# Optimization experiments

Measured on AMD Instinct MI355X. Metric: run time of the kernel, lower is better.

Reference implementation:

```python
import jax, jax.numpy as jnp
import numpy as np
from jax import lax

B, H, W, C = 16, 32, 32, 256
HEADS = 8
HD = C // HEADS          # attention_head_dim = 32
KSZ = 3                  # conv_kernel_size
DIL = 2                  # dilation_rate
SCALE = HD ** -0.5


def setup_inputs() -> dict:
    key = jax.random.key(0)
    k0, k1, k2, k3 = jax.random.split(key, 4)
    return {
        "query": jax.random.normal(k0, (B, H, W, C), jnp.float32),
        "key_in": jax.random.normal(k1, (B, H, W, C), jnp.float32),
        "value": jax.random.normal(k2, (B, H, W, C), jnp.float32),
        # depthwise conv: kernel [kh, kw, in_ch/groups=1, out_ch=C], plus bias [C]
        "conv_kernel": jax.random.normal(k3, (KSZ, KSZ, 1, C), jnp.float32) * 0.05,
        "conv_bias": jnp.zeros((C,), jnp.float32),
    }


def _dwconv(x, kernel, bias):
    # depthwise dilated conv, padding SAME (Keras Conv2D groups=C)
    y = lax.conv_general_dilated(
        x, kernel,
        window_strides=(1, 1), padding="SAME",
        rhs_dilation=(DIL, DIL),
        dimension_numbers=("NHWC", "HWIO", "NHWC"),
        feature_group_count=C,
    )
    return y + bias


def _to_heads(x):
    # [B,H,W,C] -> [B, heads, S, head_dim]
    return x.reshape(B, H * W, HEADS, HD).transpose(0, 2, 1, 3)


def reference(query, key_in, value, conv_kernel, conv_bias):
    q = _to_heads(query)
    k = _to_heads(_dwconv(key_in, conv_kernel, conv_bias))
    v = _to_heads(_dwconv(value, conv_kernel, conv_bias))
    scores = jnp.einsum("bhqd,bhkd->bhqk", q, k) * SCALE  # [B,heads,S,S]
    attn = jax.nn.softmax(scores, axis=-1)
    out = jnp.einsum("bhqk,bhkd->bhqd", attn, v)          # [B,heads,S,hd]
    return out.transpose(0, 2, 1, 3).reshape(B, H, W, C)
```

## Files before the change

### kernel.cpp

```cpp
#include <hip/hip_runtime.h>

#define B_    16
#define HH    32
#define WW    32
#define CC    256
#define HEADS 8
#define HD    32
#define S_    1024
#define KT    128
#define NITER (S_ / KT)
#define SCALE_L2E 0.25503486f

typedef unsigned short u16;
typedef unsigned int   u32;
typedef __attribute__((ext_vector_type(8))) short short8;
typedef __attribute__((ext_vector_type(4))) float f32x4;

__device__ __forceinline__ u16 f2bf(float f) {
    u32 x = __float_as_uint(f);
    return (u16)((x + 0x7fffu + ((x >> 16) & 1u)) >> 16);
}
__device__ __forceinline__ u32 pack2bf(float lo, float hi) {
    return (u32)f2bf(lo) | ((u32)f2bf(hi) << 16);
}

__global__ __launch_bounds__(256) void dw_conv_kernel(
    const float* __restrict__ key_in, const float* __restrict__ value,
    const float* __restrict__ ck, const float* __restrict__ cb,
    u16* __restrict__ Kws, u16* __restrict__ Vws)
{
    int idx = blockIdx.x * 256 + threadIdx.x;
    int c4 = idx & 63;
    int x  = (idx >> 6) & 31;
    int y  = (idx >> 11) & 31;
    int b  = (idx >> 16) & 15;
    int t  = idx >> 20;
    const float* __restrict__ src = t ? value : key_in;

    float4 acc = *(const float4*)(cb + 4 * c4);
    #pragma unroll
    for (int kh = 0; kh < 3; kh++) {
        int yy = y + kh * 2 - 2;
        if (yy < 0 || yy >= HH) continue;
        #pragma unroll
        for (int kw = 0; kw < 3; kw++) {
            int xx = x + kw * 2 - 2;
            if (xx < 0 || xx >= WW) continue;
            float4 w = *(const float4*)(ck + (kh * 3 + kw) * CC + 4 * c4);
            size_t ii = ((((size_t)b * HH + yy) * WW) + xx) * CC + 4 * c4;
            float4 v = *(const float4*)(src + ii);
            acc.x += w.x * v.x; acc.y += w.y * v.y;
            acc.z += w.z * v.z; acc.w += w.w * v.w;
        }
    }

    int h = c4 >> 3;
    int d = (c4 & 7) * 4;
    int s = y * WW + x;
    size_t o = (((size_t)(b * HEADS + h)) * S_ + s) * HD + d;
    if (t == 0) {
        *(uint2*)&Kws[o] = make_uint2(pack2bf(acc.x * SCALE_L2E, acc.y * SCALE_L2E),
                                      pack2bf(acc.z * SCALE_L2E, acc.w * SCALE_L2E));
    } else {
        *(uint2*)&Vws[o] = make_uint2(pack2bf(acc.x, acc.y), pack2bf(acc.z, acc.w));
    }
}

__global__ __launch_bounds__(256, 4) void attn_kernel(
    const float* __restrict__ query,
    const u16* __restrict__ Kws, const u16* __restrict__ Vws,
    float* __restrict__ out)
{
    __shared__ __align__(16) u16 Vtlds[2][HD][KT + 8];

    const int tid  = threadIdx.x;
    const int lane = tid & 63;
    const int wv   = tid >> 6;
    const int q15  = lane & 15;
    const int quad = lane >> 4;

    const int blk = blockIdx.x;
    const int bh  = blk & 127;
    const int qt  = blk >> 7;
    const int b = bh >> 3, h = bh & 7;
    const int q0w = qt * 128 + wv * 32;

    short8 qf[2];
    #pragma unroll
    for (int f = 0; f < 2; f++) {
        const float* qp = query + ((size_t)(b * S_ + q0w + f * 16 + q15)) * CC
                          + h * HD + quad * 8;
        float4 a = *(const float4*)(qp);
        float4 c = *(const float4*)(qp + 4);
        short8 v;
        v[0] = (short)f2bf(a.x); v[1] = (short)f2bf(a.y);
        v[2] = (short)f2bf(a.z); v[3] = (short)f2bf(a.w);
        v[4] = (short)f2bf(c.x); v[5] = (short)f2bf(c.y);
        v[6] = (short)f2bf(c.z); v[7] = (short)f2bf(c.w);
        qf[f] = v;
    }

    short8 ones;
    #pragma unroll
    for (int j = 0; j < 8; j++) ones[j] = (short)0x3F80;

    const u16* Kg = Kws + (size_t)bh * S_ * HD;
    const u16* Vg = Vws + (size_t)bh * S_ * HD;

    const int vg  = tid >> 3, vs4 = tid & 7;
    const int vc = vg >> 3, vw = vg & 7;
    const int vt2 = (vw >> 2) & 1, vqd = vw & 3;
    const int vpg = (vc << 5) | (vqd << 3) | (vt2 << 2);

    uint2 vr0, vr1, vr2, vr3;

    auto issue_v_loads = [&](int kt0) {
        const uint2* vsrc = (const uint2*)(Vg + (size_t)(kt0 + 4 * vg) * HD + 4 * vs4);
        vr0 = vsrc[0]; vr1 = vsrc[8]; vr2 = vsrc[16]; vr3 = vsrc[24];
    };
    auto write_lds = [&](int p) {
        u32 a, bb;
        a  = __builtin_amdgcn_perm(vr1.x, vr0.x, 0x05040100u);
        bb = __builtin_amdgcn_perm(vr3.x, vr2.x, 0x05040100u);
        *(uint2*)&Vtlds[p][4 * vs4 + 0][vpg] = make_uint2(a, bb);
        a  = __builtin_amdgcn_perm(vr1.x, vr0.x, 0x07060302u);
        bb = __builtin_amdgcn_perm(vr3.x, vr2.x, 0x07060302u);
        *(uint2*)&Vtlds[p][4 * vs4 + 1][vpg] = make_uint2(a, bb);
        a  = __builtin_amdgcn_perm(vr1.y, vr0.y, 0x05040100u);
        bb = __builtin_amdgcn_perm(vr3.y, vr2.y, 0x05040100u);
        *(uint2*)&Vtlds[p][4 * vs4 + 2][vpg] = make_uint2(a, bb);
        a  = __builtin_amdgcn_perm(vr1.y, vr0.y, 0x07060302u);
        bb = __builtin_amdgcn_perm(vr3.y, vr2.y, 0x07060302u);
        *(uint2*)&Vtlds[p][4 * vs4 + 3][vpg] = make_uint2(a, bb);
    };

    f32x4 Ot[2][2];
    f32x4 Dsum[2];
    #pragma unroll
    for (int f = 0; f < 2; f++) {
        Ot[f][0] = (f32x4)0.f; Ot[f][1] = (f32x4)0.f; Dsum[f] = (f32x4)0.f;
    }

    issue_v_loads(0);
    write_lds(0);

    for (int it = 0; it < NITER; it++) {
        const int p = it & 1;
        const int kt0 = it * KT;

        short8 kfr0[4], kfr1[4];
        #pragma unroll
        for (int c = 0; c < 4; c++) {
            kfr0[c] = *(const short8*)(Kg + (size_t)(kt0 + c * 32 + q15) * HD + quad * 8);
            kfr1[c] = *(const short8*)(Kg + (size_t)(kt0 + c * 32 + 16 + q15) * HD + quad * 8);
        }
        if (it + 1 < NITER) issue_v_loads((it + 1) * KT);
        __syncthreads();

        #pragma unroll
        for (int c = 0; c < 4; c++) {
            short8 vf0 = *(const short8*)&Vtlds[p][q15][c * 32 + quad * 8];
            short8 vf1 = *(const short8*)&Vtlds[p][16 + q15][c * 32 + quad * 8];
            #pragma unroll
            for (int f = 0; f < 2; f++) {
                f32x4 s0 = __builtin_amdgcn_mfma_f32_16x16x32_bf16(kfr0[c], qf[f], (f32x4)0.f, 0, 0, 0);
                f32x4 s1 = __builtin_amdgcn_mfma_f32_16x16x32_bf16(kfr1[c], qf[f], (f32x4)0.f, 0, 0, 0);
                #pragma unroll
                for (int r = 0; r < 4; r++) {
                    s0[r] = __builtin_amdgcn_exp2f(s0[r]);
                    s1[r] = __builtin_amdgcn_exp2f(s1[r]);
                }
                union { u32 u[4]; short8 s8; } pk;
                pk.u[0] = __builtin_amdgcn_perm(__float_as_uint(s0[1]),
                                                __float_as_uint(s0[0]), 0x07060302u);
                pk.u[1] = __builtin_amdgcn_perm(__float_as_uint(s0[3]),
                                                __float_as_uint(s0[2]), 0x07060302u);
                pk.u[2] = __builtin_amdgcn_perm(__float_as_uint(s1[1]),
                                                __float_as_uint(s1[0]), 0x07060302u);
                pk.u[3] = __builtin_amdgcn_perm(__float_as_uint(s1[3]),
                                                __float_as_uint(s1[2]), 0x07060302u);
                Ot[f][0] = __builtin_amdgcn_mfma_f32_16x16x32_bf16(vf0, pk.s8, Ot[f][0], 0, 0, 0);
                Ot[f][1] = __builtin_amdgcn_mfma_f32_16x16x32_bf16(vf1, pk.s8, Ot[f][1], 0, 0, 0);
                Dsum[f]  = __builtin_amdgcn_mfma_f32_16x16x32_bf16(ones, pk.s8, Dsum[f], 0, 0, 0);
            }
        }
        if (it + 1 < NITER) write_lds((it + 1) & 1);
    }

    #pragma unroll
    for (int f = 0; f < 2; f++) {
        float inv = 1.0f / Dsum[f][0];
        int qg = q0w + f * 16 + q15;
        float* op = out + ((size_t)(b * S_ + qg)) * CC + h * HD;
        #pragma unroll
        for (int h2 = 0; h2 < 2; h2++)
            #pragma unroll
            for (int r = 0; r < 4; r++)
                op[h2 * 16 + quad * 4 + r] = Ot[f][h2][r] * inv;
    }
}

extern "C" void kernel_launch(void* const* d_in, const int* in_sizes, int n_in,
                              void* d_out, int out_size, void* d_ws, size_t ws_size,
                              hipStream_t stream)
{
    const float* query  = (const float*)d_in[0];
    const float* key_in = (const float*)d_in[1];
    const float* value  = (const float*)d_in[2];
    const float* ck     = (const float*)d_in[3];
    const float* cb     = (const float*)d_in[4];
    float* out = (float*)d_out;

    u16* Kws = (u16*)d_ws;
    u16* Vws = Kws + (size_t)B_ * HEADS * S_ * HD;

    dw_conv_kernel<<<(2 * B_ * HH * WW * (CC / 4)) / 256, 256, 0, stream>>>(
        key_in, value, ck, cb, Kws, Vws);

    attn_kernel<<<(B_ * HEADS * S_) / 128, 256, 0, stream>>>(
        query, Kws, Vws, out);
}
```

Baseline: 133.8 us.

## Tile depthwise conv through LDS with a halo and per-thread register weights

The depthwise dilated conv kernel now has each block stage an 8-row output tile plus a 2-row halo for one 32-channel group into shared memory. It then computes 8 outputs per thread from LDS, with the 9 filter taps held in registers. The goal is to remove the repeated 9x global reads of input and weights in the old one-output-per-thread kernel. The costs are 48 KB of LDS per block, fewer blocks (1024), and a barrier. The attention kernel, which likely dominates runtime, is unchanged.

```diff
diff --git a/kernel.cpp b/kernel.cpp
--- a/kernel.cpp
+++ b/kernel.cpp
@@ -29,40 +29,61 @@
     const float* __restrict__ ck, const float* __restrict__ cb,
     u16* __restrict__ Kws, u16* __restrict__ Vws)
 {
-    int idx = blockIdx.x * 256 + threadIdx.x;
-    int c4 = idx & 63;
-    int x  = (idx >> 6) & 31;
-    int y  = (idx >> 11) & 31;
-    int b  = (idx >> 16) & 15;
-    int t  = idx >> 20;
-    const float* __restrict__ src = t ? value : key_in;
-
-    float4 acc = *(const float4*)(cb + 4 * c4);
-    #pragma unroll
-    for (int kh = 0; kh < 3; kh++) {
-        int yy = y + kh * 2 - 2;
-        if (yy < 0 || yy >= HH) continue;
-        #pragma unroll
-        for (int kw = 0; kw < 3; kw++) {
-            int xx = x + kw * 2 - 2;
-            if (xx < 0 || xx >= WW) continue;
-            float4 w = *(const float4*)(ck + (kh * 3 + kw) * CC + 4 * c4);
-            size_t ii = ((((size_t)b * HH + yy) * WW) + xx) * CC + 4 * c4;
-            float4 v = *(const float4*)(src + ii);
-            acc.x += w.x * v.x; acc.y += w.y * v.y;
-            acc.z += w.z * v.z; acc.w += w.w * v.w;
+    __shared__ float4 tile[3072];
+
+    const int tid = threadIdx.x;
+    const int blk = blockIdx.x;
+    const int g  = blk & 7;
+    const int yt = (blk >> 3) & 3;
+    const int b  = (blk >> 5) & 15;
+    const int t  = blk >> 9;
+    const float4* __restrict__ src4 = (const float4*)(t ? value : key_in);
+    const int y0 = yt * 8;
+
+    #pragma unroll
+    for (int i = 0; i < 12; i++) {
+        int slot = tid + i * 256;
+        int r = slot >> 8, x = (slot >> 3) & 31, cc = slot & 7;
+        int yy = y0 - 2 + r;
+        float4 v = make_float4(0.f, 0.f, 0.f, 0.f);
+        if (yy >= 0 && yy < HH)
+            v = src4[(((size_t)b * HH + yy) * WW + x) * 64 + g * 8 + cc];
+        tile[slot] = v;
+    }
+
+    const int c = tid & 7;
+    float4 w9[9];
+    #pragma unroll
+    for (int j = 0; j < 9; j++)
+        w9[j] = *(const float4*)(ck + j * CC + g * 32 + c * 4);
+    const float4 bias = *(const float4*)(cb + g * 32 + c * 4);
+
+    __syncthreads();
+
+    #pragma unroll
+    for (int i = 0; i < 8; i++) {
+        int o = tid + i * 256;
+        int x = (o >> 3) & 31, ry = o >> 8;
+        float4 acc = bias;
+        #pragma unroll
+        for (int kh = 0; kh < 3; kh++) {
+            #pragma unroll
+            for (int kw = 0; kw < 3; kw++) {
+                int xx = x - 2 + 2 * kw;
+                if (xx < 0 || xx >= WW) continue;
+                float4 v = tile[((ry + 2 * kh) * 32 + xx) * 8 + c];
+                float4 w = w9[kh * 3 + kw];
+                acc.x += w.x * v.x; acc.y += w.y * v.y;
+                acc.z += w.z * v.z; acc.w += w.w * v.w;
+            }
         }
-    }
-
-    int h = c4 >> 3;
-    int d = (c4 & 7) * 4;
-    int s = y * WW + x;
-    size_t o = (((size_t)(b * HEADS + h)) * S_ + s) * HD + d;
-    if (t == 0) {
-        *(uint2*)&Kws[o] = make_uint2(pack2bf(acc.x * SCALE_L2E, acc.y * SCALE_L2E),
-                                      pack2bf(acc.z * SCALE_L2E, acc.w * SCALE_L2E));
-    } else {
-        *(uint2*)&Vws[o] = make_uint2(pack2bf(acc.x, acc.y), pack2bf(acc.z, acc.w));
+        int spix = (y0 + ry) * WW + x;
+        size_t off = (((size_t)(b * HEADS + g)) * S_ + spix) * HD + c * 4;
+        if (t == 0)
+            *(uint2*)&Kws[off] = make_uint2(pack2bf(acc.x * SCALE_L2E, acc.y * SCALE_L2E),
+                                            pack2bf(acc.z * SCALE_L2E, acc.w * SCALE_L2E));
+        else
+            *(uint2*)&Vws[off] = make_uint2(pack2bf(acc.x, acc.y), pack2bf(acc.z, acc.w));
     }
 }
 
@@ -214,7 +235,7 @@
     u16* Kws = (u16*)d_ws;
     u16* Vws = Kws + (size_t)B_ * HEADS * S_ * HD;
 
-    dw_conv_kernel<<<(2 * B_ * HH * WW * (CC / 4)) / 256, 256, 0, stream>>>(
+    dw_conv_kernel<<<1024, 256, 0, stream>>>(
         key_in, value, ck, cb, Kws, Vws);
 
     attn_kernel<<<(B_ * HEADS * S_) / 128, 256, 0, stream>>>(
```

After: 128.4 us. 1.04x faster.
